# Kernel tuning notes

Measured on AMD Instinct MI355X. Metric: run time of the kernel, lower is better.

Reference implementation:

```python
import jax, jax.numpy as jnp
import numpy as np

EMBED_DIM = 256
UNITS = 512


def setup_inputs() -> dict:
    key = jax.random.key(0)
    k1, k2, k3, k4, k5, k6, k7, k8 = jax.random.split(key, 8)
    B, L = 2048, 64
    features = jax.random.normal(k1, (B, L, EMBED_DIM), dtype=jnp.float32)
    hidden = jax.random.normal(k2, (B, UNITS), dtype=jnp.float32)
    s1 = 1.0 / np.sqrt(EMBED_DIM)
    s2 = 1.0 / np.sqrt(UNITS)
    W1 = jax.random.normal(k3, (EMBED_DIM, UNITS), dtype=jnp.float32) * s1
    b1 = jnp.zeros((UNITS,), dtype=jnp.float32)
    W2 = jax.random.normal(k4, (UNITS, UNITS), dtype=jnp.float32) * s2
    b2 = jnp.zeros((UNITS,), dtype=jnp.float32)
    V = jax.random.normal(k5, (UNITS, 1), dtype=jnp.float32) * s2
    bV = jnp.zeros((1,), dtype=jnp.float32)
    return {"features": features, "hidden": hidden, "W1": W1, "b1": b1,
            "W2": W2, "b2": b2, "V": V, "bV": bV}


def reference(features, hidden, W1, b1, W2, b2, V, bV):
    # features: [B, L, D_feat]; hidden: [B, U]
    # score = tanh(W1(features) + W2(hidden)[:, None])  -> [B, L, U]
    proj_f = jnp.einsum('bld,du->blu', features, W1) + b1
    proj_h = hidden @ W2 + b2                         # [B, U]
    score = jnp.tanh(proj_f + proj_h[:, None, :])     # [B, L, U]
    logits = jnp.einsum('blu,uo->blo', score, V) + bV  # [B, L, 1]
    attention_weights = jax.nn.softmax(logits, axis=1)  # softmax over L
    context_vector = jnp.sum(attention_weights * features, axis=1)  # [B, D_feat]
    return context_vector, attention_weights
```

## Files before the change

kernel.cpp:

```cpp
#include <hip/hip_runtime.h>
#include <math.h>

#define B_N 2048
#define L_N 64
#define D_N 256
#define U_N 512
#define NB  8

typedef __attribute__((ext_vector_type(8))) short bf16x8;
typedef __attribute__((ext_vector_type(4))) float f32x4;

__device__ __forceinline__ float fast_tanh(float x) {
    float e = __builtin_amdgcn_exp2f(x * 2.8853900817779268f);
    float r = __builtin_amdgcn_rcpf(e + 1.0f);
    return fmaf(-2.0f, r, 1.0f);
}
__device__ __forceinline__ ushort f2bf(float x) {
    uint b = __float_as_uint(x);
    uint r = (b + 0x7FFF + ((b >> 16) & 1)) >> 16;
    return (ushort)r;
}
__device__ __forceinline__ float bf2f(ushort u) {
    uint v = ((uint)u) << 16;
    return __uint_as_float(v);
}

__global__ __launch_bounds__(256) void pack_weights(
    const float* __restrict__ W1, const float* __restrict__ W2,
    ushort* __restrict__ W1p, ushort* __restrict__ W2p)
{
    ushort tmp[8];
    if (blockIdx.x < 64) {
        int g = blockIdx.x * 256 + threadIdx.x;
        int ntg = g >> 9, ks = (g >> 6) & 7, lane = g & 63;
        int n  = ntg * 16 + (lane & 15);
        int kb = ks * 32 + (lane >> 4) * 8;
#pragma unroll
        for (int j = 0; j < 8; ++j) tmp[j] = f2bf(W1[(kb + j) * U_N + n]);
        *(uint4*)&W1p[(size_t)g * 8] = *(uint4*)tmp;
    } else {
        int g = (blockIdx.x - 64) * 256 + threadIdx.x;
        int ntg = g >> 10, ks = (g >> 6) & 15, lane = g & 63;
        int n  = ntg * 16 + (lane & 15);
        int kb = ks * 32 + (lane >> 4) * 8;
#pragma unroll
        for (int j = 0; j < 8; ++j) tmp[j] = f2bf(W2[(kb + j) * U_N + n]);
        *(uint4*)&W2p[(size_t)g * 8] = *(uint4*)tmp;
    }
}

__global__ __launch_bounds__(256) void proj_h_mfma(
    const float* __restrict__ hidden, const ushort* __restrict__ W2p,
    const float* __restrict__ b1, const float* __restrict__ b2,
    ushort* __restrict__ ph)
{
    __shared__ ushort As[16 * 512];

    const int t  = threadIdx.x;
    const int b0 = blockIdx.x * 16;
    const int u0 = blockIdx.y * 128;

#pragma unroll
    for (int i = 0; i < 4; ++i) {
        int f = t + i * 256;
        int m = f >> 6, c = f & 63;
        float4 x0 = *(const float4*)&hidden[(b0 + m) * U_N + c * 8];
        float4 x1 = *(const float4*)&hidden[(b0 + m) * U_N + c * 8 + 4];
        ushort tmp[8] = {f2bf(x0.x), f2bf(x0.y), f2bf(x0.z), f2bf(x0.w),
                         f2bf(x1.x), f2bf(x1.y), f2bf(x1.z), f2bf(x1.w)};
        *(uint4*)&As[(m * 64 + (c ^ (m & 7))) * 8] = *(uint4*)tmp;
    }
    __syncthreads();

    const int w = t >> 6, lane = t & 63;
    const int ml = lane & 15, q = lane >> 4;

    f32x4 acc[2];
#pragma unroll
    for (int nt = 0; nt < 2; ++nt) acc[nt] = (f32x4){0.f, 0.f, 0.f, 0.f};

    for (int ks = 0; ks < 16; ++ks) {
        int c = ks * 4 + q;
        bf16x8 a = *(const bf16x8*)&As[(ml * 64 + (c ^ (ml & 7))) * 8];
        bf16x8 bb[2];
#pragma unroll
        for (int nt = 0; nt < 2; ++nt) {
            int ntg = blockIdx.y * 8 + w * 2 + nt;
            bb[nt] = *(const bf16x8*)&W2p[(size_t)((ntg * 16 + ks) * 64 + lane) * 8];
        }
#pragma unroll
        for (int nt = 0; nt < 2; ++nt)
            acc[nt] = __builtin_amdgcn_mfma_f32_16x16x32_bf16(a, bb[nt], acc[nt], 0, 0, 0);
    }

#pragma unroll
    for (int nt = 0; nt < 2; ++nt) {
        int n = u0 + (w * 2 + nt) * 16 + ml;
        float bias = b1[n] + b2[n];
#pragma unroll
        for (int r = 0; r < 4; ++r)
            ph[(size_t)(b0 + q * 4 + r) * U_N + n] = f2bf(acc[nt][r] + bias);
    }
}

__global__ __launch_bounds__(512) void attn_kernel(
    const float* __restrict__ features, const ushort* __restrict__ W1p,
    const float* __restrict__ V, const float* __restrict__ bV,
    const ushort* __restrict__ ph, float* __restrict__ out)
{
    __shared__ ushort As[2][64 * 256];
    __shared__ float lpart[8][64];
    __shared__ float ctxp[2][256];
    __shared__ float wls[64];

    const int t    = threadIdx.x;
    const int w    = t >> 6;
    const int lane = t & 63;
    const int ml   = lane & 15;
    const int q    = lane >> 4;
    const int b0   = blockIdx.x * NB;

    float4 pa0, pa1, pb0, pb1;

#define ISSUE_HALF(bb, i0) do {                                               \
        const float* fb_ = features + (size_t)(bb) * (L_N * D_N);             \
        { int ch_ = t + (i0) * 512; int m_ = ch_ >> 5, cc_ = ch_ & 31;        \
          const float* s_ = &fb_[m_ * D_N + (cc_ ^ (m_ & 31)) * 8];           \
          pa0 = *(const float4*)s_; pa1 = *(const float4*)(s_ + 4); }         \
        { int ch_ = t + (i0 + 1) * 512; int m_ = ch_ >> 5, cc_ = ch_ & 31;    \
          const float* s_ = &fb_[m_ * D_N + (cc_ ^ (m_ & 31)) * 8];           \
          pb0 = *(const float4*)s_; pb1 = *(const float4*)(s_ + 4); }         \
    } while (0)

#define WRITE_HALF(buf, i0) do {                                              \
        { int ch_ = t + (i0) * 512; int m_ = ch_ >> 5, cc_ = ch_ & 31;        \
          ushort tv_[8] = {f2bf(pa0.x), f2bf(pa0.y), f2bf(pa0.z), f2bf(pa0.w),\
                           f2bf(pa1.x), f2bf(pa1.y), f2bf(pa1.z), f2bf(pa1.w)};\
          *(uint4*)&As[buf][((m_ * 32 + cc_)) * 8] = *(uint4*)tv_; }          \
        { int ch_ = t + (i0 + 1) * 512; int m_ = ch_ >> 5, cc_ = ch_ & 31;    \
          ushort tv_[8] = {f2bf(pb0.x), f2bf(pb0.y), f2bf(pb0.z), f2bf(pb0.w),\
                           f2bf(pb1.x), f2bf(pb1.y), f2bf(pb1.z), f2bf(pb1.w)};\
          *(uint4*)&As[buf][((m_ * 32 + cc_)) * 8] = *(uint4*)tv_; }          \
    } while (0)

#define KSTEP(ks) do {                                                        \
        if ((ks) < 7) {                                                       \
            _Pragma("unroll")                                                 \
            for (int nt = 0; nt < 4; ++nt)                                    \
                bfn[nt] = *(const bf16x8*)&W1w[(size_t)((nt * 8 + (ks) + 1) * 64 + lane) * 8]; \
        }                                                                     \
        bf16x8 a_[4];                                                         \
        _Pragma("unroll")                                                     \
        for (int mt = 0; mt < 4; ++mt) {                                      \
            int m_ = mt * 16 + ml, c_ = (ks) * 4 + q;                         \
            a_[mt] = *(const bf16x8*)&As[cur][(m_ * 32 + (c_ ^ (m_ & 31))) * 8]; \
        }                                                                     \
        _Pragma("unroll")                                                     \
        for (int nt = 0; nt < 4; ++nt)                                        \
            _Pragma("unroll")                                                 \
            for (int mt = 0; mt < 4; ++mt)                                    \
                acc[mt][nt] = __builtin_amdgcn_mfma_f32_16x16x32_bf16(        \
                    a_[mt], bfc[nt], acc[mt][nt], 0, 0, 0);                   \
        if ((ks) < 7) {                                                       \
            _Pragma("unroll")                                                 \
            for (int nt = 0; nt < 4; ++nt) bfc[nt] = bfn[nt];                 \
        }                                                                     \
    } while (0)

    ISSUE_HALF(b0, 0);
    WRITE_HALF(0, 0);
    ISSUE_HALF(b0, 2);
    WRITE_HALF(0, 2);
    __syncthreads();

    const ushort* W1w = W1p + (size_t)(w * 4) * 8 * 64 * 8;
    int cur = 0;

    for (int bi = 0; bi < NB; ++bi) {
        const int b = b0 + bi;
        const bool pre = (bi + 1 < NB);

        if (pre) ISSUE_HALF(b + 1, 0);
        __builtin_amdgcn_sched_barrier(0);

        f32x4 acc[4][4];
#pragma unroll
        for (int mt = 0; mt < 4; ++mt)
#pragma unroll
            for (int nt = 0; nt < 4; ++nt)
                acc[mt][nt] = (f32x4){0.f, 0.f, 0.f, 0.f};

        bf16x8 bfc[4], bfn[4];
#pragma unroll
        for (int nt = 0; nt < 4; ++nt)
            bfc[nt] = *(const bf16x8*)&W1w[(size_t)((nt * 8) * 64 + lane) * 8];

        KSTEP(0); KSTEP(1); KSTEP(2); KSTEP(3);

        if (pre) {
            WRITE_HALF(cur ^ 1, 0);
            ISSUE_HALF(b + 1, 2);
        }
        __builtin_amdgcn_sched_barrier(0);

        KSTEP(4); KSTEP(5); KSTEP(6); KSTEP(7);

        float lp[16];
#pragma unroll
        for (int j = 0; j < 16; ++j) lp[j] = 0.f;
#pragma unroll
        for (int nt = 0; nt < 4; ++nt) {
            int n = w * 64 + nt * 16 + ml;
            float phv = bf2f(ph[(size_t)b * U_N + n]);
            float vv  = V[n];
#pragma unroll
            for (int mt = 0; mt < 4; ++mt)
#pragma unroll
                for (int r = 0; r < 4; ++r) {
                    float s = fast_tanh(acc[mt][nt][r] + phv);
                    lp[mt * 4 + r] = fmaf(s, vv, lp[mt * 4 + r]);
                }
        }

#pragma unroll
        for (int off = 1; off <= 8; off <<= 1)
#pragma unroll
            for (int j = 0; j < 16; ++j)
                lp[j] += __shfl_xor(lp[j], off);

        if (pre) WRITE_HALF(cur ^ 1, 2);

        if (ml == 0) {
#pragma unroll
            for (int mt = 0; mt < 4; ++mt)
#pragma unroll
                for (int r = 0; r < 4; ++r)
                    lpart[w][mt * 16 + q * 4 + r] = lp[mt * 4 + r];
        }
        __syncthreads();

        if (t < 64) {
            float lsum = bV[0];
#pragma unroll
            for (int ww = 0; ww < 8; ++ww) lsum += lpart[ww][t];
            float mx = lsum;
#pragma unroll
            for (int off = 32; off > 0; off >>= 1)
                mx = fmaxf(mx, __shfl_xor(mx, off));
            float e = __expf(lsum - mx);
            float ssum = e;
#pragma unroll
            for (int off = 32; off > 0; off >>= 1)
                ssum += __shfl_xor(ssum, off);
            float wt = e / ssum;
            wls[t] = wt;
            out[(size_t)B_N * D_N + (size_t)b * L_N + t] = wt;
        }
        __syncthreads();

        {
            int d = t & 255, h = t >> 8;
            float cx = 0.f;
#pragma unroll 8
            for (int li = 0; li < 32; ++li) {
                int l = h * 32 + li;
                ushort u = As[cur][(l * 32 + ((d >> 3) ^ (l & 31))) * 8 + (d & 7)];
                cx = fmaf(wls[l], bf2f(u), cx);
            }
            ctxp[h][d] = cx;
        }
        __syncthreads();

        if (t < 256) out[(size_t)b * D_N + t] = ctxp[0][t] + ctxp[1][t];

        cur ^= 1;
    }
#undef ISSUE_HALF
#undef WRITE_HALF
#undef KSTEP
}

extern "C" void kernel_launch(void* const* d_in, const int* in_sizes, int n_in,
                              void* d_out, int out_size, void* d_ws, size_t ws_size,
                              hipStream_t stream) {
    const float* features = (const float*)d_in[0];
    const float* hidden   = (const float*)d_in[1];
    const float* W1       = (const float*)d_in[2];
    const float* b1       = (const float*)d_in[3];
    const float* W2       = (const float*)d_in[4];
    const float* b2       = (const float*)d_in[5];
    const float* V        = (const float*)d_in[6];
    const float* bV       = (const float*)d_in[7];
    float* out = (float*)d_out;

    ushort* ph  = (ushort*)d_ws;
    ushort* W1p = (ushort*)((char*)d_ws + (size_t)B_N * U_N * 2);
    ushort* W2p = (ushort*)((char*)d_ws + (size_t)B_N * U_N * 2 + (size_t)D_N * U_N * 2);

    pack_weights<<<192, 256, 0, stream>>>(W1, W2, W1p, W2p);
    proj_h_mfma<<<dim3(B_N / 16, U_N / 128), 256, 0, stream>>>(hidden, W2p, b1, b2, ph);
    attn_kernel<<<B_N / NB, 512, 0, stream>>>(features, W1p, V, bV, ph, out);
}
```

Baseline: 303.4 us.

## Split feature prefetch into quarter stages and drop W1 fragment double-buffering

The next batch's features were prefetched in two halves, each using two float4 pairs. They are now prefetched in four quarters, each using a single float4 pair, interleaved between every two K-steps with sched barriers. The last quarter is written before the tanh/logit epilogue. The W1 B-fragment double buffer (bfc/bfn) is replaced by per-step loads, and the MFMA loop is reordered to consume each A fragment immediately. The aim is to lower register pressure and spread global-load latency more evenly, at the risk of exposing W1 load latency inside each K-step.

```diff
diff --git a/kernel.cpp b/kernel.cpp
--- a/kernel.cpp
+++ b/kernel.cpp
@@ -120,57 +120,57 @@
     const int q    = lane >> 4;
     const int b0   = blockIdx.x * NB;
 
-    float4 pa0, pa1, pb0, pb1;
-
-#define ISSUE_HALF(bb, i0) do {                                               \
-        const float* fb_ = features + (size_t)(bb) * (L_N * D_N);             \
-        { int ch_ = t + (i0) * 512; int m_ = ch_ >> 5, cc_ = ch_ & 31;        \
-          const float* s_ = &fb_[m_ * D_N + (cc_ ^ (m_ & 31)) * 8];           \
-          pa0 = *(const float4*)s_; pa1 = *(const float4*)(s_ + 4); }         \
-        { int ch_ = t + (i0 + 1) * 512; int m_ = ch_ >> 5, cc_ = ch_ & 31;    \
-          const float* s_ = &fb_[m_ * D_N + (cc_ ^ (m_ & 31)) * 8];           \
-          pb0 = *(const float4*)s_; pb1 = *(const float4*)(s_ + 4); }         \
-    } while (0)
-
-#define WRITE_HALF(buf, i0) do {                                              \
-        { int ch_ = t + (i0) * 512; int m_ = ch_ >> 5, cc_ = ch_ & 31;        \
-          ushort tv_[8] = {f2bf(pa0.x), f2bf(pa0.y), f2bf(pa0.z), f2bf(pa0.w),\
-                           f2bf(pa1.x), f2bf(pa1.y), f2bf(pa1.z), f2bf(pa1.w)};\
-          *(uint4*)&As[buf][((m_ * 32 + cc_)) * 8] = *(uint4*)tv_; }          \
-        { int ch_ = t + (i0 + 1) * 512; int m_ = ch_ >> 5, cc_ = ch_ & 31;    \
-          ushort tv_[8] = {f2bf(pb0.x), f2bf(pb0.y), f2bf(pb0.z), f2bf(pb0.w),\
-                           f2bf(pb1.x), f2bf(pb1.y), f2bf(pb1.z), f2bf(pb1.w)};\
-          *(uint4*)&As[buf][((m_ * 32 + cc_)) * 8] = *(uint4*)tv_; }          \
+    float4 pa0, pa1;
+    float4 pb0, pb1;
+
+#define ISSUE_Q(bb_, iq) do {                                                 \
+        const float* fb_ = features + (size_t)(bb_) * (L_N * D_N);            \
+        int ch_ = t + (iq) * 512; int m_ = ch_ >> 5, cc_ = ch_ & 31;          \
+        const float* s_ = &fb_[m_ * D_N + (cc_ ^ (m_ & 31)) * 8];             \
+        pa0 = *(const float4*)s_; pa1 = *(const float4*)(s_ + 4);             \
+    } while (0)
+
+#define WRITE_Q(buf, iq) do {                                                 \
+        int ch_ = t + (iq) * 512; int m_ = ch_ >> 5, cc_ = ch_ & 31;          \
+        ushort tv_[8] = {f2bf(pa0.x), f2bf(pa0.y), f2bf(pa0.z), f2bf(pa0.w),  \
+                         f2bf(pa1.x), f2bf(pa1.y), f2bf(pa1.z), f2bf(pa1.w)}; \
+        *(uint4*)&As[buf][(m_ * 32 + cc_) * 8] = *(uint4*)tv_;                \
+    } while (0)
+
+#define ISSUE_QB(bb_, iq) do {                                                \
+        const float* fb_ = features + (size_t)(bb_) * (L_N * D_N);            \
+        int ch_ = t + (iq) * 512; int m_ = ch_ >> 5, cc_ = ch_ & 31;          \
+        const float* s_ = &fb_[m_ * D_N + (cc_ ^ (m_ & 31)) * 8];             \
+        pb0 = *(const float4*)s_; pb1 = *(const float4*)(s_ + 4);             \
+    } while (0)
+
+#define WRITE_QB(buf, iq) do {                                                \
+        int ch_ = t + (iq) * 512; int m_ = ch_ >> 5, cc_ = ch_ & 31;          \
+        ushort tv_[8] = {f2bf(pb0.x), f2bf(pb0.y), f2bf(pb0.z), f2bf(pb0.w),  \
+                         f2bf(pb1.x), f2bf(pb1.y), f2bf(pb1.z), f2bf(pb1.w)}; \
+        *(uint4*)&As[buf][(m_ * 32 + cc_) * 8] = *(uint4*)tv_;                \
     } while (0)
 
 #define KSTEP(ks) do {                                                        \
-        if ((ks) < 7) {                                                       \
-            _Pragma("unroll")                                                 \
-            for (int nt = 0; nt < 4; ++nt)                                    \
-                bfn[nt] = *(const bf16x8*)&W1w[(size_t)((nt * 8 + (ks) + 1) * 64 + lane) * 8]; \
-        }                                                                     \
-        bf16x8 a_[4];                                                         \
+        bf16x8 bb[4];                                                         \
+        _Pragma("unroll")                                                     \
+        for (int nt = 0; nt < 4; ++nt)                                        \
+            bb[nt] = *(const bf16x8*)&W1w[(size_t)((nt * 8 + (ks)) * 64 + lane) * 8]; \
         _Pragma("unroll")                                                     \
         for (int mt = 0; mt < 4; ++mt) {                                      \
             int m_ = mt * 16 + ml, c_ = (ks) * 4 + q;                         \
-            a_[mt] = *(const bf16x8*)&As[cur][(m_ * 32 + (c_ ^ (m_ & 31))) * 8]; \
+            bf16x8 av = *(const bf16x8*)&As[cur][(m_ * 32 + (c_ ^ (m_ & 31))) * 8]; \
+            _Pragma("unroll")                                                 \
+            for (int nt = 0; nt < 4; ++nt)                                    \
+                acc[mt][nt] = __builtin_amdgcn_mfma_f32_16x16x32_bf16(        \
+                    av, bb[nt], acc[mt][nt], 0, 0, 0);                        \
         }                                                                     \
-        _Pragma("unroll")                                                     \
-        for (int nt = 0; nt < 4; ++nt)                                        \
-            _Pragma("unroll")                                                 \
-            for (int mt = 0; mt < 4; ++mt)                                    \
-                acc[mt][nt] = __builtin_amdgcn_mfma_f32_16x16x32_bf16(        \
-                    a_[mt], bfc[nt], acc[mt][nt], 0, 0, 0);                   \
-        if ((ks) < 7) {                                                       \
-            _Pragma("unroll")                                                 \
-            for (int nt = 0; nt < 4; ++nt) bfc[nt] = bfn[nt];                 \
-        }                                                                     \
-    } while (0)
-
-    ISSUE_HALF(b0, 0);
-    WRITE_HALF(0, 0);
-    ISSUE_HALF(b0, 2);
-    WRITE_HALF(0, 2);
+    } while (0)
+
+    ISSUE_Q(b0, 0); ISSUE_QB(b0, 1);
+    WRITE_Q(0, 0);  WRITE_QB(0, 1);
+    ISSUE_Q(b0, 2); ISSUE_QB(b0, 3);
+    WRITE_Q(0, 2);  WRITE_QB(0, 3);
     __syncthreads();
 
     const ushort* W1w = W1p + (size_t)(w * 4) * 8 * 64 * 8;
@@ -180,9 +180,6 @@
         const int b = b0 + bi;
         const bool pre = (bi + 1 < NB);
 
-        if (pre) ISSUE_HALF(b + 1, 0);
-        __builtin_amdgcn_sched_barrier(0);
-
         f32x4 acc[4][4];
 #pragma unroll
         for (int mt = 0; mt < 4; ++mt)
@@ -190,20 +187,19 @@
             for (int nt = 0; nt < 4; ++nt)
                 acc[mt][nt] = (f32x4){0.f, 0.f, 0.f, 0.f};
 
-        bf16x8 bfc[4], bfn[4];
-#pragma unroll
-        for (int nt = 0; nt < 4; ++nt)
-            bfc[nt] = *(const bf16x8*)&W1w[(size_t)((nt * 8) * 64 + lane) * 8];
-
-        KSTEP(0); KSTEP(1); KSTEP(2); KSTEP(3);
-
-        if (pre) {
-            WRITE_HALF(cur ^ 1, 0);
-            ISSUE_HALF(b + 1, 2);
-        }
-        __builtin_amdgcn_sched_barrier(0);
-
-        KSTEP(4); KSTEP(5); KSTEP(6); KSTEP(7);
+        if (pre) ISSUE_Q(b + 1, 0);
+        __builtin_amdgcn_sched_barrier(0);
+        KSTEP(0); KSTEP(1);
+        if (pre) { WRITE_Q(cur ^ 1, 0); ISSUE_Q(b + 1, 1); }
+        __builtin_amdgcn_sched_barrier(0);
+        KSTEP(2); KSTEP(3);
+        if (pre) { WRITE_Q(cur ^ 1, 1); ISSUE_Q(b + 1, 2); }
+        __builtin_amdgcn_sched_barrier(0);
+        KSTEP(4); KSTEP(5);
+        if (pre) { WRITE_Q(cur ^ 1, 2); ISSUE_Q(b + 1, 3); }
+        __builtin_amdgcn_sched_barrier(0);
+        KSTEP(6); KSTEP(7);
+        if (pre) WRITE_Q(cur ^ 1, 3);
 
         float lp[16];
 #pragma unroll
@@ -227,8 +223,6 @@
 #pragma unroll
             for (int j = 0; j < 16; ++j)
                 lp[j] += __shfl_xor(lp[j], off);
-
-        if (pre) WRITE_HALF(cur ^ 1, 2);
 
         if (ml == 0) {
 #pragma unroll
@@ -275,8 +269,10 @@
 
         cur ^= 1;
     }
-#undef ISSUE_HALF
-#undef WRITE_HALF
+#undef ISSUE_Q
+#undef WRITE_Q
+#undef ISSUE_QB
+#undef WRITE_QB
 #undef KSTEP
 }
 
```

New measurement: 295.5 us. 2.6% less time.

## Prefetch feature tiles via global_load_lds DMA into fp32 staging buffer

Applied to the files above, without the earlier changes.

Replaces the register-staged prefetch of the next batch's features (split into two halves interleaved with MFMA k-steps) with direct global-to-LDS loads into a 64KB fp32 staging buffer. Each wave then converts its rows to bf16 into the swizzled double buffer at the end of the iteration, behind an extra barrier. It also hoists the V and bV loads out of the loop, prefetches the ph values early, and drops the register double-buffering of W1 fragments in the k-steps. This frees registers and overlaps the feature loads with compute. The costs are a large LDS footprint (64KB plus 64KB) that likely limits the kernel to one block per CU, an added full synchronisation, and a serialized convert phase.

```diff
diff --git a/kernel.cpp b/kernel.cpp
--- a/kernel.cpp
+++ b/kernel.cpp
@@ -23,6 +23,13 @@
 __device__ __forceinline__ float bf2f(ushort u) {
     uint v = ((uint)u) << 16;
     return __uint_as_float(v);
+}
+
+__device__ __forceinline__ void gll16(const ushort* g, ushort* l) {
+    __builtin_amdgcn_global_load_lds(
+        (const __attribute__((address_space(1))) unsigned int*)g,
+        (__attribute__((address_space(3))) unsigned int*)l,
+        16, 0, 0);
 }
 
 __global__ __launch_bounds__(256) void pack_weights(
@@ -108,6 +115,7 @@
     const float* __restrict__ V, const float* __restrict__ bV,
     const ushort* __restrict__ ph, float* __restrict__ out)
 {
+    __shared__ float  S[L_N * D_N];
     __shared__ ushort As[2][64 * 256];
     __shared__ float lpart[8][64];
     __shared__ float ctxp[2][256];
@@ -120,57 +128,49 @@
     const int q    = lane >> 4;
     const int b0   = blockIdx.x * NB;
 
-    float4 pa0, pa1, pb0, pb1;
-
-#define ISSUE_HALF(bb, i0) do {                                               \
-        const float* fb_ = features + (size_t)(bb) * (L_N * D_N);             \
-        { int ch_ = t + (i0) * 512; int m_ = ch_ >> 5, cc_ = ch_ & 31;        \
-          const float* s_ = &fb_[m_ * D_N + (cc_ ^ (m_ & 31)) * 8];           \
-          pa0 = *(const float4*)s_; pa1 = *(const float4*)(s_ + 4); }         \
-        { int ch_ = t + (i0 + 1) * 512; int m_ = ch_ >> 5, cc_ = ch_ & 31;    \
-          const float* s_ = &fb_[m_ * D_N + (cc_ ^ (m_ & 31)) * 8];           \
-          pb0 = *(const float4*)s_; pb1 = *(const float4*)(s_ + 4); }         \
+#define ISSUE_DMA(bb_) do {                                                   \
+        const float* fsrc_ = features + (size_t)(bb_) * (L_N * D_N) + w * 2048; \
+        _Pragma("unroll")                                                     \
+        for (int i_ = 0; i_ < 8; ++i_)                                        \
+            gll16((const ushort*)(fsrc_ + i_ * 256 + lane * 4),               \
+                  (ushort*)&S[w * 2048 + i_ * 256]);                          \
     } while (0)
 
-#define WRITE_HALF(buf, i0) do {                                              \
-        { int ch_ = t + (i0) * 512; int m_ = ch_ >> 5, cc_ = ch_ & 31;        \
-          ushort tv_[8] = {f2bf(pa0.x), f2bf(pa0.y), f2bf(pa0.z), f2bf(pa0.w),\
-                           f2bf(pa1.x), f2bf(pa1.y), f2bf(pa1.z), f2bf(pa1.w)};\
-          *(uint4*)&As[buf][((m_ * 32 + cc_)) * 8] = *(uint4*)tv_; }          \
-        { int ch_ = t + (i0 + 1) * 512; int m_ = ch_ >> 5, cc_ = ch_ & 31;    \
-          ushort tv_[8] = {f2bf(pb0.x), f2bf(pb0.y), f2bf(pb0.z), f2bf(pb0.w),\
-                           f2bf(pb1.x), f2bf(pb1.y), f2bf(pb1.z), f2bf(pb1.w)};\
-          *(uint4*)&As[buf][((m_ * 32 + cc_)) * 8] = *(uint4*)tv_; }          \
+#define CONVERT(buf) do {                                                     \
+        _Pragma("unroll")                                                     \
+        for (int i_ = 0; i_ < 8; ++i_) {                                      \
+            float4 x_ = *(const float4*)&S[w * 2048 + i_ * 256 + lane * 4];   \
+            ushort tv_[4] = {f2bf(x_.x), f2bf(x_.y), f2bf(x_.z), f2bf(x_.w)}; \
+            int m_ = w * 8 + i_, c_ = lane >> 1;                              \
+            *(uint2*)&As[buf][(m_ * 32 + (c_ ^ (m_ & 31))) * 8 + (lane & 1) * 4] \
+                = *(uint2*)tv_;                                               \
+        }                                                                     \
     } while (0)
 
 #define KSTEP(ks) do {                                                        \
-        if ((ks) < 7) {                                                       \
+        bf16x8 bb[4];                                                         \
+        _Pragma("unroll")                                                     \
+        for (int nt = 0; nt < 4; ++nt)                                        \
+            bb[nt] = *(const bf16x8*)&W1w[(size_t)((nt * 8 + (ks)) * 64 + lane) * 8]; \
+        _Pragma("unroll")                                                     \
+        for (int mt = 0; mt < 4; ++mt) {                                      \
+            int m_ = mt * 16 + ml, c_ = (ks) * 4 + q;                         \
+            bf16x8 av = *(const bf16x8*)&As[cur][(m_ * 32 + (c_ ^ (m_ & 31))) * 8]; \
             _Pragma("unroll")                                                 \
             for (int nt = 0; nt < 4; ++nt)                                    \
-                bfn[nt] = *(const bf16x8*)&W1w[(size_t)((nt * 8 + (ks) + 1) * 64 + lane) * 8]; \
-        }                                                                     \
-        bf16x8 a_[4];                                                         \
-        _Pragma("unroll")                                                     \
-        for (int mt = 0; mt < 4; ++mt) {                                      \
-            int m_ = mt * 16 + ml, c_ = (ks) * 4 + q;                         \
-            a_[mt] = *(const bf16x8*)&As[cur][(m_ * 32 + (c_ ^ (m_ & 31))) * 8]; \
-        }                                                                     \
-        _Pragma("unroll")                                                     \
-        for (int nt = 0; nt < 4; ++nt)                                        \
-            _Pragma("unroll")                                                 \
-            for (int mt = 0; mt < 4; ++mt)                                    \
                 acc[mt][nt] = __builtin_amdgcn_mfma_f32_16x16x32_bf16(        \
-                    a_[mt], bfc[nt], acc[mt][nt], 0, 0, 0);                   \
-        if ((ks) < 7) {                                                       \
-            _Pragma("unroll")                                                 \
-            for (int nt = 0; nt < 4; ++nt) bfc[nt] = bfn[nt];                 \
+                    av, bb[nt], acc[mt][nt], 0, 0, 0);                        \
         }                                                                     \
     } while (0)
 
-    ISSUE_HALF(b0, 0);
-    WRITE_HALF(0, 0);
-    ISSUE_HALF(b0, 2);
-    WRITE_HALF(0, 2);
+    float vv4[4];
+#pragma unroll
+    for (int nt = 0; nt < 4; ++nt) vv4[nt] = V[w * 64 + nt * 16 + ml];
+    const float bV0 = bV[0];
+
+    ISSUE_DMA(b0);
+    asm volatile("s_waitcnt vmcnt(0)" ::: "memory");
+    CONVERT(0);
     __syncthreads();
 
     const ushort* W1w = W1p + (size_t)(w * 4) * 8 * 64 * 8;
@@ -180,8 +180,13 @@
         const int b = b0 + bi;
         const bool pre = (bi + 1 < NB);
 
-        if (pre) ISSUE_HALF(b + 1, 0);
+        if (pre) ISSUE_DMA(b + 1);
         __builtin_amdgcn_sched_barrier(0);
+
+        ushort phu[4];
+#pragma unroll
+        for (int nt = 0; nt < 4; ++nt)
+            phu[nt] = ph[(size_t)b * U_N + w * 64 + nt * 16 + ml];
 
         f32x4 acc[4][4];
 #pragma unroll
@@ -190,19 +195,7 @@
             for (int nt = 0; nt < 4; ++nt)
                 acc[mt][nt] = (f32x4){0.f, 0.f, 0.f, 0.f};
 
-        bf16x8 bfc[4], bfn[4];
-#pragma unroll
-        for (int nt = 0; nt < 4; ++nt)
-            bfc[nt] = *(const bf16x8*)&W1w[(size_t)((nt * 8) * 64 + lane) * 8];
-
         KSTEP(0); KSTEP(1); KSTEP(2); KSTEP(3);
-
-        if (pre) {
-            WRITE_HALF(cur ^ 1, 0);
-            ISSUE_HALF(b + 1, 2);
-        }
-        __builtin_amdgcn_sched_barrier(0);
-
         KSTEP(4); KSTEP(5); KSTEP(6); KSTEP(7);
 
         float lp[16];
@@ -210,9 +203,8 @@
         for (int j = 0; j < 16; ++j) lp[j] = 0.f;
 #pragma unroll
         for (int nt = 0; nt < 4; ++nt) {
-            int n = w * 64 + nt * 16 + ml;
-            float phv = bf2f(ph[(size_t)b * U_N + n]);
-            float vv  = V[n];
+            float phv = bf2f(phu[nt]);
+            float vv  = vv4[nt];
 #pragma unroll
             for (int mt = 0; mt < 4; ++mt)
 #pragma unroll
@@ -228,8 +220,6 @@
             for (int j = 0; j < 16; ++j)
                 lp[j] += __shfl_xor(lp[j], off);
 
-        if (pre) WRITE_HALF(cur ^ 1, 2);
-
         if (ml == 0) {
 #pragma unroll
             for (int mt = 0; mt < 4; ++mt)
@@ -240,7 +230,7 @@
         __syncthreads();
 
         if (t < 64) {
-            float lsum = bV[0];
+            float lsum = bV0;
 #pragma unroll
             for (int ww = 0; ww < 8; ++ww) lsum += lpart[ww][t];
             float mx = lsum;
@@ -273,10 +263,15 @@
 
         if (t < 256) out[(size_t)b * D_N + t] = ctxp[0][t] + ctxp[1][t];
 
+        if (pre) {
+            asm volatile("s_waitcnt vmcnt(0)" ::: "memory");
+            CONVERT(cur ^ 1);
+        }
+        __syncthreads();
         cur ^= 1;
     }
-#undef ISSUE_HALF
-#undef WRITE_HALF
+#undef ISSUE_DMA
+#undef CONVERT
 #undef KSTEP
 }
 
```

After: 281.4 us. 7.3% less time.
